# Optimization experiments

Hardware: AMD Instinct MI355X
Metric: run time of the kernel (lower is better)

Reference implementation:

```python
import jax, jax.numpy as jnp
import numpy as np

K = 10          # n_near
BN_EPS = 1e-5   # BatchNorm eps; running stats at init: mean=0, var=1


def knn_idx(xt, k):
    # xt: [b, n, c] -> [b, n, k] indices of k nearest (incl. self)
    sq = jnp.sum(xt * xt, axis=-1)                               # [b, n]
    d = sq[:, :, None] - 2.0 * jnp.einsum('bnc,bmc->bnm', xt, xt) + sq[:, None, :]
    return jax.lax.top_k(-d, k)[1]                               # [b, n, k]


def graph_feature(x, k):
    # x: [b, c, n] -> [b, 2c, n, k]  (DGCNN edge features)
    xt = x.transpose(0, 2, 1)                                    # [b, n, c]
    idx = knn_idx(xt, k)                                         # [b, n, k]
    nei = jnp.take_along_axis(xt[:, None, :, :], idx[..., None], axis=2)  # [b, n, k, c]
    cen = xt[:, :, None, :]                                      # [b, n, 1, c]
    feat = jnp.concatenate([nei - cen, jnp.broadcast_to(cen, nei.shape)], axis=-1)
    return feat.transpose(0, 3, 1, 2)                            # [b, 2c, n, k]


def conv_bn_act(x, w, b, g, t):
    # 1x1 conv (any spatial rank) + inference BatchNorm (mean=0, var=1) + GELU
    sh = (1, -1) + (1,) * (x.ndim - 2)
    y = jnp.einsum('oi,bi...->bo...', w, x) + b.reshape(sh)
    y = y * (g.reshape(sh) / jnp.sqrt(1.0 + BN_EPS)) + t.reshape(sh)
    return jax.nn.gelu(y)


def setup_inputs() -> dict:
    key = jax.random.key(0)
    ks = jax.random.split(key, 8)
    d = {'x': jax.random.normal(ks[0], (8, 64, 2048), jnp.float32)}
    dims = {'11': (152, 128), '12': (181, 152), '21': (430, 362),
            '22': (512, 430), '31': (595, 693), '32': (512, 595)}
    for i, (tag, (o, inp)) in enumerate(dims.items()):
        d['w' + tag] = jax.random.normal(jax.random.fold_in(key, i + 1), (o, inp), jnp.float32) * 0.02
        d['b' + tag] = jnp.zeros((o,), jnp.float32)
        d['g' + tag] = jnp.ones((o,), jnp.float32)
        d['t' + tag] = jnp.zeros((o,), jnp.float32)
    return d


def reference(x, w11, b11, g11, t11, w12, b12, g12, t12,
              w21, b21, g21, t21, w22, b22, g22, t22,
              w31, b31, g31, t31, w32, b32, g32, t32):
    f = graph_feature(x, K)                       # [b, 128, n, k]
    f = conv_bn_act(f, w11, b11, g11, t11)
    f = conv_bn_act(f, w12, b12, g12, t12)        # [b, 181, n, k]
    x1 = jnp.max(f, axis=-1)                      # [b, 181, n]
    f = graph_feature(x1, K)                      # [b, 362, n, k]
    f = conv_bn_act(f, w21, b21, g21, t21)
    f = conv_bn_act(f, w22, b22, g22, t22)        # [b, 512, n, k]
    x2 = jnp.max(f, axis=-1)                      # [b, 512, n]
    f = jnp.concatenate([x1, x2], axis=1)         # [b, 693, n]
    f = conv_bn_act(f, w31, b31, g31, t31)
    f = conv_bn_act(f, w32, b32, g32, t32)        # [b, 512, n]
    return f
```

## Files before the change

### kernel.cpp

```cpp
#include <hip/hip_runtime.h>


typedef float f4 __attribute__((ext_vector_type(4)));
typedef float f32x4 __attribute__((ext_vector_type(4)));
typedef short bf16x8 __attribute__((ext_vector_type(8)));

#define BNRSQ 0.9999950000374997f

__device__ __forceinline__ float gelu_f(float x){
  float a = 0.7978845608028654f * (x + 0.044715f * x * x * x);
  float e = __expf(2.0f * a);
  float t = 1.0f - 2.0f / (e + 1.0f);
  return 0.5f * x * (1.0f + t);
}

__device__ __forceinline__ short f2b(float x){
  unsigned u = __float_as_uint(x);
  unsigned r = (u + 0x7fffu + ((u >> 16) & 1u)) >> 16;
  return (short)r;
}
__device__ __forceinline__ float b2f(short s){
  return __uint_as_float(((unsigned)(unsigned short)s) << 16);
}

__global__ void prep_k(const float* __restrict__ w11, const float* __restrict__ w12,
                       const float* __restrict__ w21, const float* __restrict__ w22,
                       const float* __restrict__ w31, const float* __restrict__ w32,
                       float* __restrict__ WaT11, float* __restrict__ WdT11,
                       float* __restrict__ Wr12, short* __restrict__ W21sb,
                       short* __restrict__ W22b, short* __restrict__ W31b,
                       short* __restrict__ W32b){
  const int bid = blockIdx.x;
  const int t = threadIdx.x;
  if (bid < 76){
    int split = bid >= 38;
    int id = (split ? bid - 38 : bid) * 256 + t;
    if (id < 64 * 152){
      int c = id / 152, o = id - c * 152;
      float w0 = w11[(size_t)o * 128 + c];
      float v = split ? (w11[(size_t)o * 128 + 64 + c] - w0) : w0;
      (split ? WdT11 : WaT11)[id] = v;
    }
  } else if (bid < 190){
    int id = (bid - 76) * 256 + t;
    if (id < 38 * 192 * 4){
      int i = id & 3, c = (id >> 2) % 192, kq = id / 768;
      int k = kq * 4 + i;
      float v = 0.f;
      if (c < 181 && k < 152) v = w12[(size_t)c * 152 + k];
      Wr12[id] = v;
    }
  } else if (bid < 1086){
    int n = bid - 190;
    if (t < 192){
      short v = 0;
      if (t < 181){
        if (n < 430) v = f2b(w21[(size_t)n * 362 + t]);
        else if (n >= 448 && n < 878){
          int m = n - 448;
          v = f2b(w21[(size_t)m * 362 + 181 + t] - w21[(size_t)m * 362 + t]);
        }
      }
      W21sb[(size_t)n * 192 + t] = v;
    }
  } else if (bid < 1598){
    int n = bid - 1086;
    for (int k = t; k < 448; k += 256){
      short v = 0;
      if (k < 430) v = f2b(w22[(size_t)n * 430 + k]);
      W22b[(size_t)n * 448 + k] = v;
    }
  } else if (bid < 2238){
    int n = bid - 1598;
    for (int k = t; k < 704; k += 256){
      short v = 0;
      if (n < 595 && k < 693) v = f2b(w31[(size_t)n * 693 + k]);
      W31b[(size_t)n * 704 + k] = v;
    }
  } else {
    int n = bid - 2238;
    for (int k = t; k < 640; k += 256){
      short v = 0;
      if (k < 595) v = f2b(w32[(size_t)n * 595 + k]);
      W32b[(size_t)n * 640 + k] = v;
    }
  }
}

__global__ __launch_bounds__(256) void transpose_k(const float* __restrict__ x, float* __restrict__ xt){
  __shared__ float tile[64][65];
  int b = blockIdx.y;
  int n0 = blockIdx.x * 64;
  int t = threadIdx.x;
  int a = t & 63, r = t >> 6;
  #pragma unroll
  for (int s = 0; s < 16; s++){
    int c = r + s * 4;
    tile[c][a] = x[((size_t)b * 64 + c) * 2048 + n0 + a];
  }
  __syncthreads();
  #pragma unroll
  for (int s = 0; s < 16; s++){
    int n = r + s * 4;
    xt[((size_t)b * 2048 + n0 + n) * 64 + a] = tile[a][n];
  }
}

__global__ __launch_bounds__(256) void sqnorm_k(const float* __restrict__ X, float* __restrict__ sq,
                                                int C, int ld, int npts){
  int gid = blockIdx.x * blockDim.x + threadIdx.x;
  int wid = gid >> 6, lane = gid & 63;
  if (wid >= npts) return;
  const float* row = X + (size_t)wid * ld;
  float s = 0.f;
  for (int c = lane; c < C; c += 64){ float v = row[c]; s += v * v; }
  #pragma unroll
  for (int off = 32; off; off >>= 1) s += __shfl_xor(s, off);
  if (lane == 0) sq[wid] = s;
}

__global__ __launch_bounds__(256) void dist_k(const float* __restrict__ X, const float* __restrict__ sq,
                                              float* __restrict__ dist, int C, int ldx){
  __shared__ float As[16][132];
  __shared__ float Bs[16][132];
  const int z = blockIdx.z;
  const float* Xb = X + (size_t)z * 2048 * ldx;
  const float* sqb = sq + (z << 11);
  float* db = dist + (size_t)z * 2048 * 2048;
  const int i0 = blockIdx.y * 128, j0 = blockIdx.x * 128;
  const int t = threadIdx.x;
  const int ti = t >> 4, tj = t & 15;
  const int r = t & 127, q8 = (t >> 7) * 8;
  float acc[2][2][4][4];
  #pragma unroll
  for (int a = 0; a < 2; a++)
    #pragma unroll
    for (int b = 0; b < 2; b++)
      #pragma unroll
      for (int u = 0; u < 4; u++)
        #pragma unroll
        for (int v = 0; v < 4; v++) acc[a][b][u][v] = 0.f;
  const float* Ag = Xb + (size_t)(i0 + r) * ldx + q8;
  const float* Bg = Xb + (size_t)(j0 + r) * ldx + q8;
  for (int c0 = 0; c0 < C; c0 += 16){
    f4 av0 = *(const f4*)(Ag + c0);
    f4 av1 = *(const f4*)(Ag + c0 + 4);
    f4 bv0 = *(const f4*)(Bg + c0);
    f4 bv1 = *(const f4*)(Bg + c0 + 4);
    __syncthreads();
    #pragma unroll
    for (int i = 0; i < 4; i++){
      As[q8 + i][r] = av0[i];  As[q8 + 4 + i][r] = av1[i];
      Bs[q8 + i][r] = bv0[i];  Bs[q8 + 4 + i][r] = bv1[i];
    }
    __syncthreads();
    #pragma unroll
    for (int k = 0; k < 16; k++){
      f4 a0 = *(const f4*)&As[k][ti * 4];
      f4 a1 = *(const f4*)&As[k][ti * 4 + 64];
      f4 b0 = *(const f4*)&Bs[k][tj * 4];
      f4 b1 = *(const f4*)&Bs[k][tj * 4 + 64];
      #pragma unroll
      for (int u = 0; u < 4; u++)
        #pragma unroll
        for (int v = 0; v < 4; v++){
          acc[0][0][u][v] += a0[u] * b0[v];
          acc[0][1][u][v] += a0[u] * b1[v];
          acc[1][0][u][v] += a1[u] * b0[v];
          acc[1][1][u][v] += a1[u] * b1[v];
        }
    }
  }
  #pragma unroll
  for (int ia = 0; ia < 2; ia++){
    #pragma unroll
    for (int u = 0; u < 4; u++){
      int i = i0 + ia * 64 + ti * 4 + u;
      float si = sqb[i];
      #pragma unroll
      for (int jb = 0; jb < 2; jb++){
        int j = j0 + jb * 64 + tj * 4;
        f4 o;
        #pragma unroll
        for (int v = 0; v < 4; v++) o[v] = si + sqb[j + v] - 2.0f * acc[ia][jb][u][v];
        *(f4*)&db[(size_t)i * 2048 + j] = o;
      }
    }
  }
}

__global__ __launch_bounds__(256) void topk_k(const float* __restrict__ dist, int* __restrict__ idxout){
  int z = blockIdx.y;
  int lane = threadIdx.x & 63;
  int row = blockIdx.x * 4 + (threadIdx.x >> 6);
  const float* d = dist + (size_t)z * 2048 * 2048 + (size_t)row * 2048;
  float v[32];
  #pragma unroll
  for (int s = 0; s < 32; s++) v[s] = d[s * 64 + lane];
  int* outp = idxout + (size_t)z * 20480 + (size_t)row * 10;
  for (int it = 0; it < 10; ++it){
    float bv = 3.0e38f; int bi = 0x7fffffff;
    #pragma unroll
    for (int s = 0; s < 32; s++){
      if (v[s] < bv){ bv = v[s]; bi = s * 64 + lane; }
    }
    #pragma unroll
    for (int off = 32; off; off >>= 1){
      float ov = __shfl_xor(bv, off);
      int   oi = __shfl_xor(bi, off);
      if (ov < bv || (ov == bv && oi < bi)){ bv = ov; bi = oi; }
    }
    #pragma unroll
    for (int s = 0; s < 32; s++) if (s * 64 + lane == bi) v[s] = 3.0e38f;
    if (lane == 0) outp[it] = bi;
  }
}

__global__ __launch_bounds__(256) void yz_k(const float* __restrict__ Amat, int C,
                                            const float* __restrict__ B1, const float* __restrict__ B2,
                                            int O, float* __restrict__ Y, float* __restrict__ Z){
  __shared__ float As[16][68];
  __shared__ float B1s[16][68];
  __shared__ float B2s[16][68];
  int m0 = blockIdx.y * 64, o0 = blockIdx.x * 64;
  int t = threadIdx.x;
  int cc = t & 15, rr = t >> 4;
  int oo = t & 63, kk = t >> 6;
  float accY[4][4], accZ[4][4];
  #pragma unroll
  for (int u = 0; u < 4; u++)
    #pragma unroll
    for (int v = 0; v < 4; v++){ accY[u][v] = 0.f; accZ[u][v] = 0.f; }
  for (int c0 = 0; c0 < C; c0 += 16){
    #pragma unroll
    for (int u = 0; u < 4; u++){
      int ii = rr + u * 16;
      As[cc][ii] = ((c0 + cc) < C) ? Amat[(size_t)(m0 + ii) * C + c0 + cc] : 0.f;
    }
    #pragma unroll
    for (int u = 0; u < 4; u++){
      int c = kk * 4 + u;
      bool ok = ((c0 + c) < C) && ((o0 + oo) < O);
      B1s[c][oo] = ok ? B1[(size_t)(c0 + c) * O + o0 + oo] : 0.f;
      B2s[c][oo] = ok ? B2[(size_t)(c0 + c) * O + o0 + oo] : 0.f;
    }
    __syncthreads();
    #pragma unroll
    for (int k = 0; k < 16; k++){
      f4 a  = *(const f4*)&As[k][rr * 4];
      f4 b1 = *(const f4*)&B1s[k][cc * 4];
      f4 b2 = *(const f4*)&B2s[k][cc * 4];
      #pragma unroll
      for (int u = 0; u < 4; u++)
        #pragma unroll
        for (int v = 0; v < 4; v++){
          accY[u][v] += a[u] * b1[v];
          accZ[u][v] += a[u] * b2[v];
        }
    }
    __syncthreads();
  }
  #pragma unroll
  for (int u = 0; u < 4; u++){
    int m = m0 + rr * 4 + u;
    #pragma unroll
    for (int v = 0; v < 4; v++){
      int o = o0 + cc * 4 + v;
      if (o < O){
        Y[(size_t)m * O + o] = accY[u][v];
        Z[(size_t)m * O + o] = accZ[u][v];
      }
    }
  }
}

__global__ __launch_bounds__(256) void fused1_k(
    const float* __restrict__ Y1, const float* __restrict__ Z1,
    const int* __restrict__ idx, const float* __restrict__ Wr12,
    const float* __restrict__ bb11, const float* __restrict__ gg11, const float* __restrict__ tt11,
    const float* __restrict__ bb12, const float* __restrict__ gg12, const float* __restrict__ tt12,
    float* __restrict__ x1t, short* __restrict__ x1b, float* __restrict__ sq2){
  __shared__ float h1[40][152];
  __shared__ int sidx[40];
  const int n0 = blockIdx.x * 4;
  const int t = threadIdx.x;
  if (t < 40) sidx[t] = idx[(size_t)n0 * 10 + t];
  __syncthreads();
  const int base = (n0 >> 11) << 11;
  {
    const int tc = t & 63, tr = t >> 6;
    for (int c = tc; c < 152; c += 64){
      float bb = bb11[c], sc = gg11[c] * BNRSQ, tb = tt11[c];
      for (int r = tr; r < 40; r += 4){
        int p = r / 10;
        int j = base + sidx[r];
        float y = Y1[(size_t)j * 152 + c] + Z1[(size_t)(n0 + p) * 152 + c];
        h1[r][c] = gelu_f((y + bb) * sc + tb);
      }
    }
  }
  __syncthreads();
  const int p = t >> 6, kh = (t >> 5) & 1, cg = t & 31;
  const int rbase = p * 10 + kh * 5;
  float acc[5][6];
  #pragma unroll
  for (int k = 0; k < 5; k++)
    #pragma unroll
    for (int j = 0; j < 6; j++) acc[k][j] = 0.f;
  for (int kq = 0; kq < 38; kq++){
    const float* wp = Wr12 + ((size_t)kq * 192 + cg) * 4;
    f4 wv[6];
    #pragma unroll
    for (int j = 0; j < 6; j++) wv[j] = *(const f4*)(wp + j * 128);
    f4 hv[5];
    #pragma unroll
    for (int k = 0; k < 5; k++) hv[k] = *(const f4*)&h1[rbase + k][kq * 4];
    #pragma unroll
    for (int k = 0; k < 5; k++)
      #pragma unroll
      for (int j = 0; j < 6; j++)
        acc[k][j] += hv[k][0] * wv[j][0] + hv[k][1] * wv[j][1]
                   + hv[k][2] * wv[j][2] + hv[k][3] * wv[j][3];
  }
  float ssum = 0.f;
  #pragma unroll
  for (int j = 0; j < 6; j++){
    int c = cg + j * 32;
    float m = 0.f;
    if (c < 181){
      float bb = bb12[c], sc = gg12[c] * BNRSQ, tb = tt12[c];
      m = -3.0e38f;
      #pragma unroll
      for (int k = 0; k < 5; k++){
        float v = gelu_f((acc[k][j] + bb) * sc + tb);
        m = fmaxf(m, v);
      }
    }
    float o = __shfl_xor(m, 32);
    m = fmaxf(m, o);
    if (kh == 0){
      float mv = (c < 181) ? m : 0.f;
      x1t[(size_t)(n0 + p) * 192 + c] = mv;
      x1b[(size_t)(n0 + p) * 192 + c] = f2b(mv);
      ssum += mv * mv;
    }
  }
  #pragma unroll
  for (int off = 16; off; off >>= 1) ssum += __shfl_xor(ssum, off);
  if (kh == 0 && cg == 0) sq2[n0 + p] = ssum;
}

__global__ __launch_bounds__(256) void h2_k(
    const float* __restrict__ YZ, const int* __restrict__ idx,
    const float* __restrict__ bb21, const float* __restrict__ gg21, const float* __restrict__ tt21,
    short* __restrict__ H2){
  __shared__ int sidx[10];
  int bl = blockIdx.x;
  int t = threadIdx.x;
  if (t < 10) sidx[t] = ((bl >> 11) << 11) + idx[(size_t)bl * 10 + t];
  __syncthreads();
  int cA = t;
  int cB = t + 256;
  float zA = YZ[(size_t)bl * 896 + 448 + cA] + bb21[cA];
  float scA = gg21[cA] * BNRSQ, tbA = tt21[cA];
  float zB = 0.f, scB = 0.f, tbB = 0.f;
  bool realB = cB < 430, padB = cB < 448;
  if (realB){
    zB = YZ[(size_t)bl * 896 + 448 + cB] + bb21[cB];
    scB = gg21[cB] * BNRSQ; tbB = tt21[cB];
  }
  #pragma unroll
  for (int k = 0; k < 10; k++){
    int nb = sidx[k];
    size_t rb = ((size_t)bl * 10 + k) * 448;
    float yA = YZ[(size_t)nb * 896 + cA] + zA;
    H2[rb + cA] = f2b(gelu_f(yA * scA + tbA));
    if (padB){
      short v = 0;
      if (realB){
        float yB = YZ[(size_t)nb * 896 + cB] + zB;
        v = f2b(gelu_f(yB * scB + tbB));
      }
      H2[rb + cB] = v;
    }
  }
}

template<int MODE>
__global__ __launch_bounds__(256) void gemm_k(const short* __restrict__ A,
                                              const short* __restrict__ Bt,
                                              int Kp, int Nld, int Nreal,
                                              const float* __restrict__ bv,
                                              const float* __restrict__ gv,
                                              const float* __restrict__ tv,
                                              void* __restrict__ outp){
  __shared__ short As[128][40];
  __shared__ short Bs[128][40];
  const int t = threadIdx.x;
  const int w = t >> 6, l = t & 63;
  const int m0 = blockIdx.y * 128, n0 = blockIdx.x * 128;
  f32x4 acc[2][8];
  #pragma unroll
  for (int i = 0; i < 2; i++)
    #pragma unroll
    for (int j = 0; j < 8; j++) acc[i][j] = (f32x4)0.f;
  const int ar = t >> 2, akc = t & 3;
  const short* Ag0 = A + (size_t)(m0 + ar) * Kp + akc * 8;
  const short* Ag1 = A + (size_t)(m0 + 64 + ar) * Kp + akc * 8;
  const short* Bg0 = Bt + (size_t)(n0 + ar) * Kp + akc * 8;
  const short* Bg1 = Bt + (size_t)(n0 + 64 + ar) * Kp + akc * 8;
  const int mrow = w * 32 + (l & 15);
  const int kg = (l >> 4) * 8;
  const int cl = l & 15;
  for (int k0 = 0; k0 < Kp; k0 += 32){
    int4 va0 = *(const int4*)(Ag0 + k0);
    int4 va1 = *(const int4*)(Ag1 + k0);
    int4 vb0 = *(const int4*)(Bg0 + k0);
    int4 vb1 = *(const int4*)(Bg1 + k0);
    __syncthreads();
    *(int4*)&As[ar][akc * 8]      = va0;
    *(int4*)&As[ar + 64][akc * 8] = va1;
    *(int4*)&Bs[ar][akc * 8]      = vb0;
    *(int4*)&Bs[ar + 64][akc * 8] = vb1;
    __syncthreads();
    bf16x8 a0 = *(const bf16x8*)&As[mrow][kg];
    bf16x8 a1 = *(const bf16x8*)&As[mrow + 16][kg];
    #pragma unroll
    for (int ni = 0; ni < 8; ni++){
      bf16x8 b = *(const bf16x8*)&Bs[cl + ni * 16][kg];
      acc[0][ni] = __builtin_amdgcn_mfma_f32_16x16x32_bf16(a0, b, acc[0][ni], 0, 0, 0);
      acc[1][ni] = __builtin_amdgcn_mfma_f32_16x16x32_bf16(a1, b, acc[1][ni], 0, 0, 0);
    }
  }
  const int rbase = (l >> 4) * 4;
  #pragma unroll
  for (int ni = 0; ni < 8; ni++){
    int n = n0 + ni * 16 + cl;
    float bb = 0.f, sc = 0.f, tb = 0.f;
    if (MODE != 2 && n < Nreal){ bb = bv[n]; sc = gv[n] * BNRSQ; tb = tv[n]; }
    #pragma unroll
    for (int mi = 0; mi < 2; mi++){
      #pragma unroll
      for (int r = 0; r < 4; r++){
        int m = m0 + w * 32 + mi * 16 + rbase + r;
        float a = acc[mi][ni][r];
        float v = (MODE == 2) ? a : gelu_f((a + bb) * sc + tb);
        if (MODE == 0) ((short*)outp)[(size_t)m * Nld + n] = f2b(v);
        else           ((float*)outp)[(size_t)m * Nld + n] = v;
      }
    }
  }
}

__global__ __launch_bounds__(256) void kmax_k(const short* __restrict__ Pb, short* __restrict__ x2b){
  int p = blockIdx.x;
  int t = threadIdx.x;
  #pragma unroll
  for (int j = 0; j < 2; j++){
    int o = t + j * 256;
    float m = -3.0e38f;
    #pragma unroll
    for (int k = 0; k < 10; k++) m = fmaxf(m, b2f(Pb[((size_t)p * 10 + k) * 512 + o]));
    x2b[(size_t)p * 512 + o] = f2b(m);
  }
}

__global__ __launch_bounds__(256) void fcat_k(const float* __restrict__ x1t, const short* __restrict__ x2b,
                                              short* __restrict__ F){
  size_t g = blockIdx.x;
  int t = threadIdx.x;
  for (int c = t; c < 704; c += 256){
    short v = 0;
    if (c < 181) v = f2b(x1t[g * 192 + c]);
    else if (c < 693) v = x2b[g * 512 + (c - 181)];
    F[g * 704 + c] = v;
  }
}

__global__ __launch_bounds__(256) void trout_k(const float* __restrict__ H6, float* __restrict__ out){
  __shared__ float tile[64][65];
  int b = blockIdx.z;
  int nc = blockIdx.x * 64, oc = blockIdx.y * 64;
  int t = threadIdx.x;
  int a = t & 63, r = t >> 6;
  #pragma unroll
  for (int s = 0; s < 16; s++){
    int nl = r + s * 4;
    tile[nl][a] = H6[((size_t)b * 2048 + nc + nl) * 512 + oc + a];
  }
  __syncthreads();
  #pragma unroll
  for (int s = 0; s < 16; s++){
    int ol = r + s * 4;
    out[((size_t)(b * 512 + oc + ol)) * 2048 + nc + a] = tile[a][ol];
  }
}

extern "C" void kernel_launch(void* const* d_in, const int* in_sizes, int n_in,
                              void* d_out, int out_size, void* d_ws, size_t ws_size,
                              hipStream_t stream) {
  const float* x   = (const float*)d_in[0];
  const float* w11 = (const float*)d_in[1];
  const float* b11 = (const float*)d_in[2];
  const float* g11 = (const float*)d_in[3];
  const float* t11 = (const float*)d_in[4];
  const float* w12 = (const float*)d_in[5];
  const float* b12 = (const float*)d_in[6];
  const float* g12 = (const float*)d_in[7];
  const float* t12 = (const float*)d_in[8];
  const float* w21 = (const float*)d_in[9];
  const float* b21 = (const float*)d_in[10];
  const float* g21 = (const float*)d_in[11];
  const float* t21 = (const float*)d_in[12];
  const float* w22 = (const float*)d_in[13];
  const float* b22 = (const float*)d_in[14];
  const float* g22 = (const float*)d_in[15];
  const float* t22 = (const float*)d_in[16];
  const float* w31 = (const float*)d_in[17];
  const float* b31 = (const float*)d_in[18];
  const float* g31 = (const float*)d_in[19];
  const float* t31 = (const float*)d_in[20];
  const float* w32 = (const float*)d_in[21];
  const float* b32 = (const float*)d_in[22];
  const float* g32 = (const float*)d_in[23];
  const float* t32 = (const float*)d_in[24];
  float* out = (float*)d_out;
  char* ws = (char*)d_ws;

  size_t off = 0;
  auto alloc = [&](size_t nbytes) -> char* {
    char* p = ws + off;
    off += ((nbytes + 255) & ~(size_t)255);
    return p;
  };
  float* x1t  = (float*)alloc((size_t)16384 * 192 * 4);
  short* x1b  = (short*)alloc((size_t)16384 * 192 * 2);
  short* x2b  = (short*)alloc((size_t)16384 * 512 * 2);
  float* sq1  = (float*)alloc(65536);
  float* sq2  = (float*)alloc(65536);
  int*   idx1 = (int*)  alloc(655360);
  int*   idx2 = (int*)  alloc(655360);
  float* WaT11 = (float*)alloc(64 * 152 * 4);
  float* WdT11 = (float*)alloc(64 * 152 * 4);
  float* Wr12  = (float*)alloc(38 * 192 * 4 * 4);
  short* W21sb = (short*)alloc((size_t)896 * 192 * 2);
  short* W22b  = (short*)alloc((size_t)512 * 448 * 2);
  short* W31b  = (short*)alloc((size_t)640 * 704 * 2);
  short* W32b  = (short*)alloc((size_t)512 * 640 * 2);
  char* arena = ws + off;
  const size_t ARENA = 93323264;
  if (off + ARENA > ws_size) return;
  float* distP = (float*)(arena);
  float* Y1    = (float*)(arena + 67108864);
  float* Z1    = (float*)(arena + 77070336);
  float* xt    = (float*)(arena + 87031808);
  short* Pb    = (short*)(arena);
  short* H2b   = (short*)(arena + 41943040);
  float* YZ2g  = (float*)(arena + 78643200);
  short* F     = (short*)(arena);
  short* H5    = (short*)(arena + 23068672);
  float* H6    = (float*)(arena + 44040192);

  prep_k<<<dim3(2750), dim3(256), 0, stream>>>(w11, w12, w21, w22, w31, w32,
                                               WaT11, WdT11, Wr12, W21sb, W22b, W31b, W32b);

  transpose_k<<<dim3(32, 8), dim3(256), 0, stream>>>(x, xt);
  sqnorm_k<<<dim3(4096), dim3(256), 0, stream>>>(xt, sq1, 64, 64, 16384);

  for (int pb = 0; pb < 2; pb++){
    dist_k<<<dim3(16, 16, 4), dim3(256), 0, stream>>>(xt + (size_t)pb * 4 * 2048 * 64,
                                                      sq1 + pb * 8192, distP, 64, 64);
    topk_k<<<dim3(512, 4), dim3(256), 0, stream>>>(distP, idx1 + (size_t)pb * 4 * 20480);
  }
  yz_k<<<dim3(3, 256), dim3(256), 0, stream>>>(xt, 64, WaT11, WdT11, 152, Y1, Z1);
  fused1_k<<<dim3(4096), dim3(256), 0, stream>>>(Y1, Z1, idx1, Wr12,
                                                 b11, g11, t11, b12, g12, t12,
                                                 x1t, x1b, sq2);

  for (int pb = 0; pb < 2; pb++){
    dist_k<<<dim3(16, 16, 4), dim3(256), 0, stream>>>(x1t + (size_t)pb * 4 * 2048 * 192,
                                                      sq2 + pb * 8192, distP, 192, 192);
    topk_k<<<dim3(512, 4), dim3(256), 0, stream>>>(distP, idx2 + (size_t)pb * 4 * 20480);
  }
  for (int g = 0; g < 4; g++){
    gemm_k<2><<<dim3(7, 32), dim3(256), 0, stream>>>(x1b + (size_t)g * 4096 * 192, W21sb,
                                                     192, 896, 896,
                                                     nullptr, nullptr, nullptr, (void*)YZ2g);
    h2_k<<<dim3(4096), dim3(256), 0, stream>>>(YZ2g, idx2 + (size_t)g * 40960,
                                               b21, g21, t21, H2b);
    gemm_k<0><<<dim3(4, 320), dim3(256), 0, stream>>>(H2b, W22b, 448, 512, 512,
                                                      b22, g22, t22, (void*)Pb);
    kmax_k<<<dim3(4096), dim3(256), 0, stream>>>(Pb, x2b + (size_t)g * 4096 * 512);
  }

  fcat_k<<<dim3(16384), dim3(256), 0, stream>>>(x1t, x2b, F);
  gemm_k<0><<<dim3(5, 128), dim3(256), 0, stream>>>(F, W31b, 704, 640, 595,
                                                    b31, g31, t31, (void*)H5);
  gemm_k<1><<<dim3(4, 128), dim3(256), 0, stream>>>(H5, W32b, 640, 512, 512,
                                                    b32, g32, t32, (void*)H6);
  trout_k<<<dim3(32, 8, 8), dim3(256), 0, stream>>>(H6, out);
}
```

Baseline: 1.080 ms.

## Fuse per-tile top-10 selection into distance kernel, merge candidates in small kernel

The distance GEMM no longer writes the full 2048x2048 distance matrix per batch. Each 128-column tile now runs a 10-round partial selection over its registers with 16-lane shuffles and emits 10 candidates per row. A new merge kernel reduces the 160 candidates per row to the final top-10. This removes large global writes and reads of the distance matrix but adds serial selection work to the GEMM epilogue.

```diff
diff --git a/kernel.cpp b/kernel.cpp
--- a/kernel.cpp
+++ b/kernel.cpp
@@ -120,13 +120,13 @@
 }
 
 __global__ __launch_bounds__(256) void dist_k(const float* __restrict__ X, const float* __restrict__ sq,
-                                              float* __restrict__ dist, int C, int ldx){
+                                              float* __restrict__ candV, int* __restrict__ candI,
+                                              int C, int ldx){
   __shared__ float As[16][132];
   __shared__ float Bs[16][132];
   const int z = blockIdx.z;
   const float* Xb = X + (size_t)z * 2048 * ldx;
   const float* sqb = sq + (z << 11);
-  float* db = dist + (size_t)z * 2048 * 2048;
   const int i0 = blockIdx.y * 128, j0 = blockIdx.x * 128;
   const int t = threadIdx.x;
   const int ti = t >> 4, tj = t & 15;
@@ -172,37 +172,74 @@
     }
   }
   #pragma unroll
-  for (int ia = 0; ia < 2; ia++){
+  for (int ia = 0; ia < 2; ia++)
     #pragma unroll
     for (int u = 0; u < 4; u++){
       int i = i0 + ia * 64 + ti * 4 + u;
       float si = sqb[i];
       #pragma unroll
-      for (int jb = 0; jb < 2; jb++){
-        int j = j0 + jb * 64 + tj * 4;
-        f4 o;
+      for (int jb = 0; jb < 2; jb++)
         #pragma unroll
-        for (int v = 0; v < 4; v++) o[v] = si + sqb[j + v] - 2.0f * acc[ia][jb][u][v];
-        *(f4*)&db[(size_t)i * 2048 + j] = o;
+        for (int v = 0; v < 4; v++){
+          int j = j0 + jb * 64 + tj * 4 + v;
+          acc[ia][jb][u][v] = si + sqb[j] - 2.0f * acc[ia][jb][u][v];
+        }
+    }
+  const int bj = blockIdx.x;
+  #pragma unroll
+  for (int ia = 0; ia < 2; ia++)
+    #pragma unroll
+    for (int u = 0; u < 4; u++){
+      int rrow = i0 + ia * 64 + ti * 4 + u;
+      unsigned alive = 0xFFu;
+      size_t cbase = (((size_t)z * 2048 + rrow) * 16 + bj) * 10;
+      for (int it = 0; it < 10; ++it){
+        float bv = 3.0e38f; int bi = 0x7fffffff;
+        #pragma unroll
+        for (int s = 0; s < 8; s++){
+          if (alive & (1u << s)){
+            int jb = s >> 2, v = s & 3;
+            float x = acc[ia][jb][u][v];
+            int xi = j0 + jb * 64 + tj * 4 + v;
+            if (x < bv || (x == bv && xi < bi)){ bv = x; bi = xi; }
+          }
+        }
+        #pragma unroll
+        for (int off = 1; off < 16; off <<= 1){
+          float ov = __shfl_xor(bv, off);
+          int   oi = __shfl_xor(bi, off);
+          if (ov < bv || (ov == bv && oi < bi)){ bv = ov; bi = oi; }
+        }
+        #pragma unroll
+        for (int s = 0; s < 8; s++){
+          int jb = s >> 2, v = s & 3;
+          if (j0 + jb * 64 + tj * 4 + v == bi) alive &= ~(1u << s);
+        }
+        if (tj == 0){ candV[cbase + it] = bv; candI[cbase + it] = bi; }
       }
     }
-  }
-}
-
-__global__ __launch_bounds__(256) void topk_k(const float* __restrict__ dist, int* __restrict__ idxout){
+}
+
+__global__ __launch_bounds__(256) void topm_k(const float* __restrict__ candV,
+                                              const int* __restrict__ candI,
+                                              int* __restrict__ idxout){
   int z = blockIdx.y;
   int lane = threadIdx.x & 63;
   int row = blockIdx.x * 4 + (threadIdx.x >> 6);
-  const float* d = dist + (size_t)z * 2048 * 2048 + (size_t)row * 2048;
-  float v[32];
-  #pragma unroll
-  for (int s = 0; s < 32; s++) v[s] = d[s * 64 + lane];
+  size_t base = ((size_t)z * 2048 + row) * 160;
+  float v[3]; int vi[3];
+  #pragma unroll
+  for (int s = 0; s < 3; s++){
+    int slot = lane + s * 64;
+    if (slot < 160){ v[s] = candV[base + slot]; vi[s] = candI[base + slot]; }
+    else { v[s] = 3.0e38f; vi[s] = 0x7fffffff; }
+  }
   int* outp = idxout + (size_t)z * 20480 + (size_t)row * 10;
   for (int it = 0; it < 10; ++it){
     float bv = 3.0e38f; int bi = 0x7fffffff;
     #pragma unroll
-    for (int s = 0; s < 32; s++){
-      if (v[s] < bv){ bv = v[s]; bi = s * 64 + lane; }
+    for (int s = 0; s < 3; s++){
+      if (v[s] < bv || (v[s] == bv && vi[s] < bi)){ bv = v[s]; bi = vi[s]; }
     }
     #pragma unroll
     for (int off = 32; off; off >>= 1){
@@ -211,7 +248,7 @@
       if (ov < bv || (ov == bv && oi < bi)){ bv = ov; bi = oi; }
     }
     #pragma unroll
-    for (int s = 0; s < 32; s++) if (s * 64 + lane == bi) v[s] = 3.0e38f;
+    for (int s = 0; s < 3; s++) if (vi[s] == bi) v[s] = 3.0e38f;
     if (lane == 0) outp[it] = bi;
   }
 }
@@ -550,7 +587,8 @@
   char* arena = ws + off;
   const size_t ARENA = 93323264;
   if (off + ARENA > ws_size) return;
-  float* distP = (float*)(arena);
+  float* candV = (float*)(arena);
+  int*   candI = (int*)  (arena + 5242880);
   float* Y1    = (float*)(arena + 67108864);
   float* Z1    = (float*)(arena + 77070336);
   float* xt    = (float*)(arena + 87031808);
@@ -569,8 +607,8 @@
 
   for (int pb = 0; pb < 2; pb++){
     dist_k<<<dim3(16, 16, 4), dim3(256), 0, stream>>>(xt + (size_t)pb * 4 * 2048 * 64,
-                                                      sq1 + pb * 8192, distP, 64, 64);
-    topk_k<<<dim3(512, 4), dim3(256), 0, stream>>>(distP, idx1 + (size_t)pb * 4 * 20480);
+                                                      sq1 + pb * 8192, candV, candI, 64, 64);
+    topm_k<<<dim3(512, 4), dim3(256), 0, stream>>>(candV, candI, idx1 + (size_t)pb * 4 * 20480);
   }
   yz_k<<<dim3(3, 256), dim3(256), 0, stream>>>(xt, 64, WaT11, WdT11, 152, Y1, Z1);
   fused1_k<<<dim3(4096), dim3(256), 0, stream>>>(Y1, Z1, idx1, Wr12,
@@ -579,8 +617,8 @@
 
   for (int pb = 0; pb < 2; pb++){
     dist_k<<<dim3(16, 16, 4), dim3(256), 0, stream>>>(x1t + (size_t)pb * 4 * 2048 * 192,
-                                                      sq2 + pb * 8192, distP, 192, 192);
-    topk_k<<<dim3(512, 4), dim3(256), 0, stream>>>(distP, idx2 + (size_t)pb * 4 * 20480);
+                                                      sq2 + pb * 8192, candV, candI, 192, 192);
+    topm_k<<<dim3(512, 4), dim3(256), 0, stream>>>(candV, candI, idx2 + (size_t)pb * 4 * 20480);
   }
   for (int g = 0; g < 4; g++){
     gemm_k<2><<<dim3(7, 32), dim3(256), 0, stream>>>(x1b + (size_t)g * 4096 * 192, W21sb,
```

After: 1.517 ms. 1.4x slower.
